# Kernel optimization log

Measured on AMD Instinct MI355X. Metric: run time of the kernel, lower is better.

The kernel has to match this reference:

```python
import jax, jax.numpy as jnp
import numpy as np
import math

D_MODEL = 2048
D_STATE = 16
EXPAND = 2
D_INNER = D_MODEL * EXPAND          # 4096
DT_RANK = math.ceil(D_MODEL / 16)   # 128
BATCH, SEQ_LEN = 2, 512


def setup_inputs() -> dict:
    key = jax.random.key(0)
    ks = jax.random.split(key, 6)
    x = jax.random.normal(ks[0], (BATCH, SEQ_LEN, D_INNER), dtype=jnp.float32)
    # A_log such that A = -exp(A_log) is a stable negative-real decay
    A_log = jnp.log(jax.random.uniform(ks[1], (D_INNER, D_STATE), minval=0.5, maxval=16.0, dtype=jnp.float32))
    D = jnp.ones((D_INNER,), dtype=jnp.float32)
    x_proj_w = 0.02 * jax.random.normal(ks[2], (DT_RANK + 2 * D_STATE, D_INNER), dtype=jnp.float32)
    dt_init_std = DT_RANK ** -0.5
    dt_proj_w = jax.random.uniform(ks[3], (D_INNER, DT_RANK), minval=-dt_init_std, maxval=dt_init_std, dtype=jnp.float32)
    # inverse-softplus init of dt bias, dt ~ loguniform[1e-3, 0.1]
    dt = jnp.exp(jax.random.uniform(ks[4], (D_INNER,), dtype=jnp.float32) * (math.log(0.1) - math.log(0.001)) + math.log(0.001))
    dt = jnp.clip(dt, 1e-4, None)
    dt_proj_b = dt + jnp.log(-jnp.expm1(-dt))
    return {"x": x, "A_log": A_log, "D": D, "x_proj_w": x_proj_w,
            "dt_proj_w": dt_proj_w, "dt_proj_b": dt_proj_b}


def reference(x, A_log, D, x_proj_w, dt_proj_w, dt_proj_b):
    # x: (b, l, d)
    A = -jnp.exp(A_log)                                  # (d, n)
    xp = jnp.einsum('bld,rd->blr', x, x_proj_w)          # (b, l, dt_rank + 2n)
    dt_in = xp[..., :DT_RANK]
    B = xp[..., DT_RANK:DT_RANK + D_STATE]               # (b, l, n)
    C = xp[..., DT_RANK + D_STATE:]                      # (b, l, n)
    dt = jax.nn.softplus(jnp.einsum('blr,dr->bld', dt_in, dt_proj_w) + dt_proj_b)  # (b, l, d)
    dA = jnp.exp(dt[..., None] * A)                      # (b, l, d, n)
    dBx = dt[..., None] * B[:, :, None, :] * x[..., None]  # (b, l, d, n)

    def step(h, inp):
        dA_t, dBx_t, C_t = inp                           # (b,d,n), (b,d,n), (b,n)
        h = dA_t * h + dBx_t
        y = jnp.einsum('bdn,bn->bd', h, C_t)
        return h, y

    h0 = jnp.zeros((x.shape[0], D_INNER, D_STATE), dtype=x.dtype)
    _, ys = jax.lax.scan(step, h0,
                         (jnp.moveaxis(dA, 1, 0), jnp.moveaxis(dBx, 1, 0), jnp.moveaxis(C, 1, 0)))
    y = jnp.moveaxis(ys, 0, 1) + D * x                   # (b, l, d)
    return y
```

## Files before the change

### kernel.cpp

```cpp
#include <hip/hip_runtime.h>
#include <math.h>

#define BATCH   2
#define SEQLEN  512
#define DI      4096
#define DS      16
#define RDT     128
#define RTOT    160
#define BL      1024

#define LOG2E 1.44269504088896340736f
#define LN2   0.69314718055994530942f

typedef __bf16 bf16;
typedef bf16  bf16x8 __attribute__((ext_vector_type(8)));
typedef float f32x4  __attribute__((ext_vector_type(4)));

__device__ __forceinline__ bf16x8 cvt8(const float4 a, const float4 b) {
  bf16x8 r;
  r[0] = (bf16)a.x; r[1] = (bf16)a.y; r[2] = (bf16)a.z; r[3] = (bf16)a.w;
  r[4] = (bf16)b.x; r[5] = (bf16)b.y; r[6] = (bf16)b.z; r[7] = (bf16)b.w;
  return r;
}

__device__ __forceinline__ bf16x8 cvt8s(const float4 a, const float4 b, const float s) {
  bf16x8 r;
  r[0] = (bf16)(s * a.x); r[1] = (bf16)(s * a.y); r[2] = (bf16)(s * a.z); r[3] = (bf16)(s * a.w);
  r[4] = (bf16)(s * b.x); r[5] = (bf16)(s * b.y); r[6] = (bf16)(s * b.z); r[7] = (bf16)(s * b.w);
  return r;
}

__global__ __launch_bounds__(256) void zero_xp(float* __restrict__ xp) {
  const int i = blockIdx.x * 256 + threadIdx.x;
  *(float4*)&xp[4 * (size_t)i] = make_float4(0.f, 0.f, 0.f, 0.f);
}

#define MT    16
#define KS    8
#define LPAD  168

__global__ __launch_bounds__(256, 2) void gemm_xp(const float* __restrict__ x,
                                                  const float* __restrict__ W,
                                                  float* __restrict__ xp) {
  __shared__ float Lred[4][MT * LPAD];
  const int tid = threadIdx.x;
  const int w = tid >> 6;
  const int lane = tid & 63;
  const int m = lane & 15;
  const int q = lane >> 4;
  const int row0 = blockIdx.x * MT;
  const int k0 = blockIdx.y * (DI / KS) + w * 128;

  f32x4 acc[10] = {};
  const float* ap = x + (size_t)(row0 + m) * DI + k0 + 8 * q;
  const float* wp = W + (size_t)m * DI + k0 + 8 * q;

#pragma unroll
  for (int kk = 0; kk < 128; kk += 32) {
    float4 a0 = *(const float4*)(ap + kk);
    float4 a1 = *(const float4*)(ap + kk + 4);
    bf16x8 af = cvt8(a0, a1);
#pragma unroll
    for (int nt = 0; nt < 10; ++nt) {
      const float* wq = wp + (size_t)nt * 16 * DI + kk;
      float4 b0 = *(const float4*)(wq);
      float4 b1 = *(const float4*)(wq + 4);
      acc[nt] = __builtin_amdgcn_mfma_f32_16x16x32_bf16(af, cvt8(b0, b1), acc[nt], 0, 0, 0);
    }
  }

#pragma unroll
  for (int nt = 0; nt < 10; ++nt)
#pragma unroll
    for (int r = 0; r < 4; ++r)
      Lred[w][(4 * q + r) * LPAD + nt * 16 + m] = acc[nt][r];
  __syncthreads();

#pragma unroll
  for (int i = 0; i < 10; ++i) {
    const int o = i * 256 + tid;
    const int row = o / 160;
    const int col = o - row * 160;
    const int a = row * LPAD + col;
    const float s = Lred[0][a] + Lred[1][a] + Lred[2][a] + Lred[3][a];
    unsafeAtomicAdd(&xp[(size_t)(row0 + row) * RTOT + col], s);
  }
}

__device__ __forceinline__ float row16_reduce_add(float p) {
  p += __int_as_float(__builtin_amdgcn_update_dpp(
      0, __float_as_int(p), 0x111, 0xf, 0xf, true));
  p += __int_as_float(__builtin_amdgcn_update_dpp(
      0, __float_as_int(p), 0x112, 0xf, 0xf, true));
  p += __int_as_float(__builtin_amdgcn_update_dpp(
      0, __float_as_int(p), 0x114, 0xf, 0xf, true));
  p += __int_as_float(__builtin_amdgcn_update_dpp(
      0, __float_as_int(p), 0x118, 0xf, 0xf, true));
  return p;
}

#define TC  64
#define TCP 68
#define NCH (SEQLEN / TC)

__global__ __launch_bounds__(256, 2) void scan_fused(const float* __restrict__ x,
                                                     const float* __restrict__ A_log,
                                                     const float* __restrict__ Dvec,
                                                     const float* __restrict__ xp,
                                                     const float* __restrict__ dtw,
                                                     const float* __restrict__ dtb,
                                                     float* __restrict__ out) {
  __shared__ __align__(16) float dtS[16][TCP];
  __shared__ __align__(16) float xS[16][TCP];
  __shared__ __align__(16) float BS[16][TCP];
  __shared__ __align__(16) float CS[16][TCP];
  __shared__ __align__(16) float yS[TC][16];

  const int bid = blockIdx.x;
  const int b = bid >> 8;
  const int d0 = (bid & 255) * 16;
  const int tid = threadIdx.x;
  const int n = tid & 15;
  const int dc = tid >> 4;
  const int d = d0 + dc;
  const int w = tid >> 6;
  const int m = tid & 15;
  const int q = (tid >> 4) & 3;

  const float A2 = -LOG2E * __expf(A_log[d * DS + n]);
  const float Dd = Dvec[d];
  const float bias2 = dtb[d0 + m] * LOG2E;

  bf16x8 bfragW[4];
#pragma unroll
  for (int k = 0; k < 4; ++k) {
    const float* p = dtw + (size_t)(d0 + m) * RDT + 32 * k + 8 * q;
    float4 w0 = *(const float4*)p;
    float4 w1 = *(const float4*)(p + 4);
    bfragW[k] = cvt8s(w0, w1, LOG2E);
  }

  const int lt = tid >> 2;
  const int lf = (tid & 3) * 4;
  const int rowbase = b * SEQLEN;

  float4 a0[4], a1[4];
  float4 rx, rB, rC;
  {
    const int arow = rowbase + 16 * w + m;
#pragma unroll
    for (int k = 0; k < 4; ++k) {
      const float* p = xp + (size_t)arow * RTOT + 32 * k + 8 * q;
      a0[k] = *(const float4*)p;
      a1[k] = *(const float4*)(p + 4);
    }
    const int row = rowbase + lt;
    rx = *(const float4*)&x[(size_t)row * DI + d0 + lf];
    rB = *(const float4*)&xp[(size_t)row * RTOT + RDT + lf];
    rC = *(const float4*)&xp[(size_t)row * RTOT + RDT + 16 + lf];
  }

  float h = 0.f;

  for (int c = 0; c < NCH; ++c) {
    if (c > 0) __syncthreads();

    {
      f32x4 acc = {};
#pragma unroll
      for (int k = 0; k < 4; ++k)
        acc = __builtin_amdgcn_mfma_f32_16x16x32_bf16(cvt8(a0[k], a1[k]), bfragW[k], acc, 0, 0, 0);
#pragma unroll
      for (int r = 0; r < 4; ++r) {
        const float z2 = acc[r] + bias2;
        dtS[m][16 * w + 4 * q + r] = (z2 > 28.854f) ? z2 * LN2
                                   : LN2 * __log2f(1.f + exp2f(z2));
      }
    }
    {
      const float rxa[4] = {rx.x, rx.y, rx.z, rx.w};
      const float rBa[4] = {rB.x, rB.y, rB.z, rB.w};
      const float rCa[4] = {rC.x, rC.y, rC.z, rC.w};
#pragma unroll
      for (int j = 0; j < 4; ++j) {
        xS[lf + j][lt] = rxa[j];
        BS[lf + j][lt] = rBa[j];
        CS[lf + j][lt] = rCa[j];
      }
    }
    if (c > 0) {
      const int prow = rowbase + (c - 1) * TC + lt;
      float4 yv = *(const float4*)&yS[lt][lf];
      *(float4*)&out[(size_t)prow * DI + d0 + lf] = yv;
    }

    __syncthreads();

    if (c < NCH - 1) {
      const int arow = rowbase + (c + 1) * TC + 16 * w + m;
#pragma unroll
      for (int k = 0; k < 4; ++k) {
        const float* p = xp + (size_t)arow * RTOT + 32 * k + 8 * q;
        a0[k] = *(const float4*)p;
        a1[k] = *(const float4*)(p + 4);
      }
      const int row = rowbase + (c + 1) * TC + lt;
      rx = *(const float4*)&x[(size_t)row * DI + d0 + lf];
      rB = *(const float4*)&xp[(size_t)row * RTOT + RDT + lf];
      rC = *(const float4*)&xp[(size_t)row * RTOT + RDT + 16 + lf];
    }

#pragma unroll
    for (int g = 0; g < 8; ++g) {
      const int t0 = 8 * g;
      const float4 dv0 = *(const float4*)&dtS[dc][t0];
      const float4 dv1 = *(const float4*)&dtS[dc][t0 + 4];
      const float4 xv0 = *(const float4*)&xS[dc][t0];
      const float4 xv1 = *(const float4*)&xS[dc][t0 + 4];
      const float4 Bv0 = *(const float4*)&BS[n][t0];
      const float4 Bv1 = *(const float4*)&BS[n][t0 + 4];
      const float4 Cv0 = *(const float4*)&CS[n][t0];
      const float4 Cv1 = *(const float4*)&CS[n][t0 + 4];
      const float dt[8] = {dv0.x, dv0.y, dv0.z, dv0.w, dv1.x, dv1.y, dv1.z, dv1.w};
      const float xv[8] = {xv0.x, xv0.y, xv0.z, xv0.w, xv1.x, xv1.y, xv1.z, xv1.w};
      const float Bv[8] = {Bv0.x, Bv0.y, Bv0.z, Bv0.w, Bv1.x, Bv1.y, Bv1.z, Bv1.w};
      const float Cv[8] = {Cv0.x, Cv0.y, Cv0.z, Cv0.w, Cv1.x, Cv1.y, Cv1.z, Cv1.w};

      float e[8], u[8], p[8];
#pragma unroll
      for (int j = 0; j < 8; ++j) {
        e[j] = exp2f(dt[j] * A2);
        u[j] = dt[j] * xv[j] * Bv[j];
      }
#pragma unroll
      for (int j = 0; j < 8; ++j) {
        h = fmaf(e[j], h, u[j]);
        p[j] = h * Cv[j];
      }
#pragma unroll
      for (int j = 0; j < 8; ++j)
        p[j] = row16_reduce_add(p[j]);
      if (n == 15) {
#pragma unroll
        for (int j = 0; j < 8; ++j)
          yS[t0 + j][dc] = fmaf(Dd, xv[j], p[j]);
      }
    }
  }

  __syncthreads();
  {
    const int prow = rowbase + (NCH - 1) * TC + lt;
    float4 yv = *(const float4*)&yS[lt][lf];
    *(float4*)&out[(size_t)prow * DI + d0 + lf] = yv;
  }
}

extern "C" void kernel_launch(void* const* d_in, const int* in_sizes, int n_in,
                              void* d_out, int out_size, void* d_ws, size_t ws_size,
                              hipStream_t stream) {
  const float* x     = (const float*)d_in[0];
  const float* A_log = (const float*)d_in[1];
  const float* Dv    = (const float*)d_in[2];
  const float* W     = (const float*)d_in[3];
  const float* dtw   = (const float*)d_in[4];
  const float* dtb   = (const float*)d_in[5];
  float* out = (float*)d_out;

  float* xp = (float*)d_ws;

  zero_xp<<<dim3(160), 256, 0, stream>>>(xp);
  gemm_xp<<<dim3(64, KS), 256, 0, stream>>>(x, W, xp);
  scan_fused<<<dim3(512), 256, 0, stream>>>(x, A_log, Dv, xp, dtw, dtb, out);
}
```

Baseline: 147.3 us.

## Drop split-K atomics, store dt_in as bf16, move D*x skip to store

The x_proj GEMM no longer splits K across 8 blocks with atomic adds into a pre-zeroed buffer. It now runs 64 blocks of 512 threads that reduce the full K in shared memory, which removes the zeroing kernel and the atomics. It writes dt_in as bf16 and B/C as separate fp32 arrays, so the scan loads pre-converted MFMA fragments. The scan also uses raw exp2/log builtins, applies the D*x skip term at output-store time, and drops the unroll pragma on the inner group loop. Only 64 GEMM blocks now run on a large GPU, which risks underutilisation of the GEMM stage.

```diff
diff --git a/kernel.cpp b/kernel.cpp
--- a/kernel.cpp
+++ b/kernel.cpp
@@ -30,33 +30,26 @@
   return r;
 }
 
-__global__ __launch_bounds__(256) void zero_xp(float* __restrict__ xp) {
-  const int i = blockIdx.x * 256 + threadIdx.x;
-  *(float4*)&xp[4 * (size_t)i] = make_float4(0.f, 0.f, 0.f, 0.f);
-}
-
-#define MT    16
-#define KS    8
-#define LPAD  168
-
-__global__ __launch_bounds__(256, 2) void gemm_xp(const float* __restrict__ x,
-                                                  const float* __restrict__ W,
-                                                  float* __restrict__ xp) {
-  __shared__ float Lred[4][MT * LPAD];
+#define LPAD 164
+
+__global__ __launch_bounds__(512) void gemm_xp1(const float* __restrict__ x,
+                                                const float* __restrict__ W,
+                                                bf16* __restrict__ dtin,
+                                                float* __restrict__ BCf) {
+  __shared__ float Lred[4][16 * LPAD];
   const int tid = threadIdx.x;
   const int w = tid >> 6;
   const int lane = tid & 63;
   const int m = lane & 15;
   const int q = lane >> 4;
-  const int row0 = blockIdx.x * MT;
-  const int k0 = blockIdx.y * (DI / KS) + w * 128;
+  const int row0 = blockIdx.x * 16;
+  const int k0 = w * 512;
 
   f32x4 acc[10] = {};
   const float* ap = x + (size_t)(row0 + m) * DI + k0 + 8 * q;
   const float* wp = W + (size_t)m * DI + k0 + 8 * q;
 
-#pragma unroll
-  for (int kk = 0; kk < 128; kk += 32) {
+  for (int kk = 0; kk < 512; kk += 32) {
     float4 a0 = *(const float4*)(ap + kk);
     float4 a1 = *(const float4*)(ap + kk + 4);
     bf16x8 af = cvt8(a0, a1);
@@ -69,21 +62,32 @@
     }
   }
 
-#pragma unroll
-  for (int nt = 0; nt < 10; ++nt)
-#pragma unroll
-    for (int r = 0; r < 4; ++r)
-      Lred[w][(4 * q + r) * LPAD + nt * 16 + m] = acc[nt][r];
+  if (w < 4) {
+#pragma unroll
+    for (int nt = 0; nt < 10; ++nt)
+#pragma unroll
+      for (int r = 0; r < 4; ++r)
+        Lred[w][(4 * q + r) * LPAD + nt * 16 + m] = acc[nt][r];
+  }
   __syncthreads();
-
-#pragma unroll
-  for (int i = 0; i < 10; ++i) {
-    const int o = i * 256 + tid;
+  if (w >= 4) {
+#pragma unroll
+    for (int nt = 0; nt < 10; ++nt)
+#pragma unroll
+      for (int r = 0; r < 4; ++r)
+        Lred[w - 4][(4 * q + r) * LPAD + nt * 16 + m] += acc[nt][r];
+  }
+  __syncthreads();
+
+#pragma unroll
+  for (int i = 0; i < 5; ++i) {
+    const int o = i * 512 + tid;
     const int row = o / 160;
     const int col = o - row * 160;
     const int a = row * LPAD + col;
     const float s = Lred[0][a] + Lred[1][a] + Lred[2][a] + Lred[3][a];
-    unsafeAtomicAdd(&xp[(size_t)(row0 + row) * RTOT + col], s);
+    if (col < RDT) dtin[(size_t)(row0 + row) * RDT + col] = (bf16)s;
+    else           BCf[(size_t)(row0 + row) * 32 + (col - RDT)] = s;
   }
 }
 
@@ -103,13 +107,14 @@
 #define TCP 68
 #define NCH (SEQLEN / TC)
 
-__global__ __launch_bounds__(256, 2) void scan_fused(const float* __restrict__ x,
-                                                     const float* __restrict__ A_log,
-                                                     const float* __restrict__ Dvec,
-                                                     const float* __restrict__ xp,
-                                                     const float* __restrict__ dtw,
-                                                     const float* __restrict__ dtb,
-                                                     float* __restrict__ out) {
+__global__ __launch_bounds__(256) void scan_fused(const float* __restrict__ x,
+                                                  const float* __restrict__ A_log,
+                                                  const float* __restrict__ Dvec,
+                                                  const float* __restrict__ BCf,
+                                                  const bf16* __restrict__ dtin,
+                                                  const float* __restrict__ dtw,
+                                                  const float* __restrict__ dtb,
+                                                  float* __restrict__ out) {
   __shared__ __align__(16) float dtS[16][TCP];
   __shared__ __align__(16) float xS[16][TCP];
   __shared__ __align__(16) float BS[16][TCP];
@@ -128,7 +133,6 @@
   const int q = (tid >> 4) & 3;
 
   const float A2 = -LOG2E * __expf(A_log[d * DS + n]);
-  const float Dd = Dvec[d];
   const float bias2 = dtb[d0 + m] * LOG2E;
 
   bf16x8 bfragW[4];
@@ -143,21 +147,19 @@
   const int lt = tid >> 2;
   const int lf = (tid & 3) * 4;
   const int rowbase = b * SEQLEN;
-
-  float4 a0[4], a1[4];
-  float4 rx, rB, rC;
+  const float4 Dv4 = *(const float4*)&Dvec[d0 + lf];
+
+  bf16x8 afrag[4];
+  float4 rx, rB, rC, rx_prev;
   {
     const int arow = rowbase + 16 * w + m;
 #pragma unroll
-    for (int k = 0; k < 4; ++k) {
-      const float* p = xp + (size_t)arow * RTOT + 32 * k + 8 * q;
-      a0[k] = *(const float4*)p;
-      a1[k] = *(const float4*)(p + 4);
-    }
+    for (int k = 0; k < 4; ++k)
+      afrag[k] = *(const bf16x8*)(dtin + (size_t)arow * RDT + 32 * k + 8 * q);
     const int row = rowbase + lt;
     rx = *(const float4*)&x[(size_t)row * DI + d0 + lf];
-    rB = *(const float4*)&xp[(size_t)row * RTOT + RDT + lf];
-    rC = *(const float4*)&xp[(size_t)row * RTOT + RDT + 16 + lf];
+    rB = *(const float4*)&BCf[row * 32 + lf];
+    rC = *(const float4*)&BCf[row * 32 + 16 + lf];
   }
 
   float h = 0.f;
@@ -169,12 +171,13 @@
       f32x4 acc = {};
 #pragma unroll
       for (int k = 0; k < 4; ++k)
-        acc = __builtin_amdgcn_mfma_f32_16x16x32_bf16(cvt8(a0[k], a1[k]), bfragW[k], acc, 0, 0, 0);
+        acc = __builtin_amdgcn_mfma_f32_16x16x32_bf16(afrag[k], bfragW[k], acc, 0, 0, 0);
 #pragma unroll
       for (int r = 0; r < 4; ++r) {
         const float z2 = acc[r] + bias2;
-        dtS[m][16 * w + 4 * q + r] = (z2 > 28.854f) ? z2 * LN2
-                                   : LN2 * __log2f(1.f + exp2f(z2));
+        dtS[m][16 * w + 4 * q + r] =
+            (z2 > 28.854f) ? z2 * LN2
+                           : LN2 * __builtin_amdgcn_logf(1.f + __builtin_amdgcn_exp2f(z2));
       }
     }
     {
@@ -191,26 +194,28 @@
     if (c > 0) {
       const int prow = rowbase + (c - 1) * TC + lt;
       float4 yv = *(const float4*)&yS[lt][lf];
-      *(float4*)&out[(size_t)prow * DI + d0 + lf] = yv;
-    }
+      float4 o4;
+      o4.x = fmaf(Dv4.x, rx_prev.x, yv.x);
+      o4.y = fmaf(Dv4.y, rx_prev.y, yv.y);
+      o4.z = fmaf(Dv4.z, rx_prev.z, yv.z);
+      o4.w = fmaf(Dv4.w, rx_prev.w, yv.w);
+      *(float4*)&out[(size_t)prow * DI + d0 + lf] = o4;
+    }
+    rx_prev = rx;
 
     __syncthreads();
 
     if (c < NCH - 1) {
       const int arow = rowbase + (c + 1) * TC + 16 * w + m;
 #pragma unroll
-      for (int k = 0; k < 4; ++k) {
-        const float* p = xp + (size_t)arow * RTOT + 32 * k + 8 * q;
-        a0[k] = *(const float4*)p;
-        a1[k] = *(const float4*)(p + 4);
-      }
+      for (int k = 0; k < 4; ++k)
+        afrag[k] = *(const bf16x8*)(dtin + (size_t)arow * RDT + 32 * k + 8 * q);
       const int row = rowbase + (c + 1) * TC + lt;
       rx = *(const float4*)&x[(size_t)row * DI + d0 + lf];
-      rB = *(const float4*)&xp[(size_t)row * RTOT + RDT + lf];
-      rC = *(const float4*)&xp[(size_t)row * RTOT + RDT + 16 + lf];
-    }
-
-#pragma unroll
+      rB = *(const float4*)&BCf[row * 32 + lf];
+      rC = *(const float4*)&BCf[row * 32 + 16 + lf];
+    }
+
     for (int g = 0; g < 8; ++g) {
       const int t0 = 8 * g;
       const float4 dv0 = *(const float4*)&dtS[dc][t0];
@@ -229,7 +234,7 @@
       float e[8], u[8], p[8];
 #pragma unroll
       for (int j = 0; j < 8; ++j) {
-        e[j] = exp2f(dt[j] * A2);
+        e[j] = __builtin_amdgcn_exp2f(dt[j] * A2);
         u[j] = dt[j] * xv[j] * Bv[j];
       }
 #pragma unroll
@@ -243,7 +248,7 @@
       if (n == 15) {
 #pragma unroll
         for (int j = 0; j < 8; ++j)
-          yS[t0 + j][dc] = fmaf(Dd, xv[j], p[j]);
+          yS[t0 + j][dc] = p[j];
       }
     }
   }
@@ -252,7 +257,12 @@
   {
     const int prow = rowbase + (NCH - 1) * TC + lt;
     float4 yv = *(const float4*)&yS[lt][lf];
-    *(float4*)&out[(size_t)prow * DI + d0 + lf] = yv;
+    float4 o4;
+    o4.x = fmaf(Dv4.x, rx_prev.x, yv.x);
+    o4.y = fmaf(Dv4.y, rx_prev.y, yv.y);
+    o4.z = fmaf(Dv4.z, rx_prev.z, yv.z);
+    o4.w = fmaf(Dv4.w, rx_prev.w, yv.w);
+    *(float4*)&out[(size_t)prow * DI + d0 + lf] = o4;
   }
 }
 
@@ -267,9 +277,10 @@
   const float* dtb   = (const float*)d_in[5];
   float* out = (float*)d_out;
 
-  float* xp = (float*)d_ws;
-
-  zero_xp<<<dim3(160), 256, 0, stream>>>(xp);
-  gemm_xp<<<dim3(64, KS), 256, 0, stream>>>(x, W, xp);
-  scan_fused<<<dim3(512), 256, 0, stream>>>(x, A_log, Dv, xp, dtw, dtb, out);
-}
+  char* ws = (char*)d_ws;
+  bf16*  dtin = (bf16*)ws;
+  float* BCf  = (float*)(ws + 262144);
+
+  gemm_xp1<<<dim3(64), 512, 0, stream>>>(x, W, dtin, BCf);
+  scan_fused<<<dim3(512), 256, 0, stream>>>(x, A_log, Dv, BCf, dtin, dtw, dtb, out);
+}
```

Result: slower. 193.7 us (+31.5%).
